# Kernel optimization log

Measured on AMD Instinct MI355X. Metric: run time of the kernel, lower is better.

The kernel has to match this reference:

```python
import jax, jax.numpy as jnp
import numpy as np

EMBED_DIM = 128
N_HEADS = 8
HEAD_DEPTH = EMBED_DIM // N_HEADS  # 16
CLIP = 10.0
B, N = 256, 1000


def setup_inputs() -> dict:
    key = jax.random.key(0)
    ks = jax.random.split(key, 10)
    D = EMBED_DIM
    return {
        "node_embeddings": jax.random.normal(ks[0], (B, N, D), jnp.float32),
        "graph_embedding": jax.random.normal(ks[1], (B, D), jnp.float32),
        "step_context": jax.random.normal(ks[2], (B, 1, D + 2), jnp.float32),
        "mask": jax.random.randint(ks[3], (B, 1, N), 0, 2).astype(bool),
        "Wk1": jax.random.normal(ks[4], (D, D), jnp.float32) / np.sqrt(D),
        "Wv": jax.random.normal(ks[5], (D, D), jnp.float32) / np.sqrt(D),
        "Wk2": jax.random.normal(ks[6], (D, D), jnp.float32) / np.sqrt(D),
        "Wq_fixed": jax.random.normal(ks[7], (D, D), jnp.float32) / np.sqrt(D),
        "Wout": jax.random.normal(ks[8], (D, D), jnp.float32) / np.sqrt(D),
        "Wq_step": jax.random.normal(ks[9], (D + 2, D), jnp.float32) / np.sqrt(D),
    }


def reference(node_embeddings, graph_embedding, step_context, mask,
              Wk1, Wv, Wk2, Wq_fixed, Wout, Wq_step):
    b, n, D = node_embeddings.shape
    H, dh = N_HEADS, HEAD_DEPTH
    neg_inf = jnp.float32(-1e9)

    # compute_static: precomputed projections of node/graph embeddings
    K1 = node_embeddings @ Wk1                      # [B,N,D]
    V = node_embeddings @ Wv                        # [B,N,D]
    K2 = node_embeddings @ Wk2                      # [B,N,D]
    Q_fixed = graph_embedding[:, None, :] @ Wq_fixed  # [B,1,D]

    # compute_dynamic: single-query masked MHA
    Q_step = step_context @ Wq_step                 # [B,1,D]
    Q1 = Q_fixed + Q_step                           # [B,1,D]
    q = Q1.reshape(b, 1, H, dh)
    k = K1.reshape(b, n, H, dh)
    v = V.reshape(b, n, H, dh)
    score = jnp.einsum('bqhd,bkhd->bhqk', q, k) / jnp.sqrt(jnp.float32(dh))
    score = jnp.where(mask[:, None, :, :], neg_inf, score)  # mask [B,1,N] -> [B,1,1,N]
    attn = jax.nn.softmax(score, axis=-1)           # [B,H,1,N]
    mha = jnp.einsum('bhqk,bkhd->bqhd', attn, v).reshape(b, 1, D)
    Q2 = mha @ Wout                                 # [B,1,D]

    # SHA: clipped single-head logits over all nodes
    logits = CLIP * jnp.tanh(
        jnp.einsum('bqd,bkd->bqk', Q2, K2) / jnp.sqrt(jnp.float32(D)))  # [B,1,N]
    logits = jnp.where(mask, neg_inf, logits)
    return logits[:, 0, :]                          # [B,N]
```

## Files before the change

### kernel.cpp

```cpp
#include <hip/hip_runtime.h>
#include <hip/hip_bf16.h>
#include <stdint.h>


#define DD 128
#define NH 8
#define DHD 16
#define NS 16
#define TILE 64
#define RP 132
#define NMAX_PAD 1024

typedef short v8s __attribute__((ext_vector_type(8)));
typedef float v4f __attribute__((ext_vector_type(4)));
typedef unsigned int v2u __attribute__((ext_vector_type(2)));

__device__ __forceinline__ unsigned short f2bf(float x) {
    unsigned u = __float_as_uint(x);
    u += 0x7fffu + ((u >> 16) & 1u);
    return (unsigned short)(u >> 16);
}
__device__ __forceinline__ float bf2f(unsigned short s) {
    return __uint_as_float((unsigned)s << 16);
}
__device__ __forceinline__ unsigned packbf2(float x, float y) {
    union { __hip_bfloat162 h; unsigned u; } cvt;
    cvt.h = __float22bfloat162_rn(make_float2(x, y));
    return cvt.u;
}

__device__ __forceinline__ v2u ds_tr16(unsigned addr) {
    v2u r;
    asm volatile("ds_read_b64_tr_b16 %0, %1" : "=v"(r) : "v"(addr));
    return r;
}
__device__ __forceinline__ v8s combine8(v2u lo, v2u hi) {
    union { struct { v2u lo, hi; } p; v8s v; } u;
    u.p.lo = lo; u.p.hi = hi;
    return u.v;
}

__device__ __forceinline__ bool detect_mask32(const void* maskp) {
    const uint32_t* mw = (const uint32_t*)maskp;
    bool m32 = true;
    #pragma unroll
    for (int i = 0; i < 16; ++i) m32 = m32 && (mw[i] <= 1u);
    return m32;
}

__global__ __launch_bounds__(128)
void k0_prep(const float* __restrict__ graph, const float* __restrict__ ctx,
             const float* __restrict__ Wk1, const float* __restrict__ Wqf,
             const float* __restrict__ Wqs, float* __restrict__ wq_ws)
{
    __shared__ float q1[DD];
    const int b = blockIdx.x, tid = threadIdx.x;
    const float* ge = graph + (size_t)b * DD;
    const float* sc = ctx + (size_t)b * (DD + 2);
    float acc = 0.f;
    #pragma unroll 4
    for (int k = 0; k < DD; ++k)     acc += ge[k] * Wqf[k * DD + tid];
    #pragma unroll 4
    for (int k = 0; k < DD + 2; ++k) acc += sc[k] * Wqs[k * DD + tid];
    q1[tid] = acc;
    __syncthreads();
    const float* wrow = Wk1 + (size_t)tid * DD;
    #pragma unroll
    for (int h = 0; h < NH; ++h) {
        float a = 0.f;
        #pragma unroll
        for (int j = 0; j < DHD; ++j) a += wrow[h * DHD + j] * q1[h * DHD + j];
        wq_ws[(size_t)b * NH * DD + h * DD + tid] = 0.25f * a;
    }
}

__global__ __launch_bounds__(256)
void kA_mfma(const float* __restrict__ node, const float* __restrict__ wq_ws,
             const void* __restrict__ maskp, unsigned short* __restrict__ spart_ws,
             float* __restrict__ mz_ws, int N)
{
    __shared__ __align__(16) unsigned short tA[8][TILE][16];
    __shared__ __align__(16) unsigned short Ph[16][72];
    __shared__ float wmax[16][5];
    __shared__ float zpart[16][5];

    const int b = blockIdx.y, j = blockIdx.x, tid = threadIdx.x;
    const int lane = tid & 63, w = tid >> 6;
    const int c = lane & 15, g = lane >> 4;
    const int rows = (N + NS - 1) / NS;
    const int n0 = j * rows;
    const int nend = min(n0 + rows, N);

    if (nend <= n0) {
        unsigned short* sp = spart_ws + ((size_t)b * NS + j) * NH * DD;
        for (int o = tid; o < NH * DD; o += 256) sp[o] = 0;
        if (tid < NH) {
            float* mzp = mz_ws + (((size_t)b * NS + j) * NH + tid) * 2;
            mzp[0] = -1e30f; mzp[1] = 0.f;
        }
        return;
    }

    const float* nodeB = node + (size_t)b * N * DD;

    const int L = tid >> 2, q = tid & 3;
    {
        const int n = n0 + L;
        const bool valid = n < nend;
        const int srcrow = valid ? n : (nend - 1);
        const float4* src = (const float4*)(nodeB + (size_t)srcrow * DD + q * 32);
        float4 f[8];
        #pragma unroll
        for (int k = 0; k < 8; ++k) f[k] = src[k];
        if (!valid) {
            #pragma unroll
            for (int k = 0; k < 8; ++k) f[k] = make_float4(0.f, 0.f, 0.f, 0.f);
        }
        union { unsigned u[16]; v8s v[4]; } pk;
        #pragma unroll
        for (int k = 0; k < 8; ++k) {
            pk.u[2 * k]     = packbf2(f[k].x, f[k].y);
            pk.u[2 * k + 1] = packbf2(f[k].z, f[k].w);
        }
        *(v8s*)&tA[2 * q][L][0]     = pk.v[0];
        *(v8s*)&tA[2 * q][L][8]     = pk.v[1];
        *(v8s*)&tA[2 * q + 1][L][0] = pk.v[2];
        *(v8s*)&tA[2 * q + 1][L][8] = pk.v[3];
    }

    v8s aw[4];
    #pragma unroll
    for (int kk = 0; kk < 4; ++kk) {
        v8s a;
        #pragma unroll
        for (int i = 0; i < 8; ++i) a[i] = 0;
        if (c < NH) {
            const float* wr = wq_ws + (size_t)b * NH * DD + (size_t)c * DD + kk * 32 + g * 8;
            #pragma unroll
            for (int i = 0; i < 8; ++i) a[i] = (short)f2bf(wr[i]);
        }
        aw[kk] = a;
    }

    const bool m32 = detect_mask32(maskp);
    const int32_t* mi = (const int32_t*)maskp + (size_t)b * N;
    const uint8_t* mb = (const uint8_t*)maskp + (size_t)b * N;

    __syncthreads();

    const int nrow = n0 + w * 16 + c;
    v4f sc = {0.f, 0.f, 0.f, 0.f};
    #pragma unroll
    for (int kk = 0; kk < 4; ++kk) {
        const v8s bfrag = *(const v8s*)&tA[2 * kk + (g >> 1)][w * 16 + c][(g & 1) * 8];
        sc = __builtin_amdgcn_mfma_f32_16x16x32_bf16(aw[kk], bfrag, sc, 0, 0, 0);
    }

    float s4[4];
    {
        const bool valid = nrow < nend;
        const bool msk = valid && (m32 ? (mi[nrow] != 0) : (mb[nrow] != 0));
        #pragma unroll
        for (int r = 0; r < 4; ++r)
            s4[r] = !valid ? -1e30f : (msk ? -1e9f : sc[r]);
    }

    {
        float mx[4];
        #pragma unroll
        for (int r = 0; r < 4; ++r) mx[r] = s4[r];
        #pragma unroll
        for (int d = 1; d < 16; d <<= 1) {
            #pragma unroll
            for (int r = 0; r < 4; ++r) mx[r] = fmaxf(mx[r], __shfl_xor(mx[r], d));
        }
        if (c == 0) {
            #pragma unroll
            for (int r = 0; r < 4; ++r) wmax[g * 4 + r][w] = mx[r];
        }
    }
    __syncthreads();

    {
        float e4[4];
        #pragma unroll
        for (int r = 0; r < 4; ++r) {
            const int h = g * 4 + r;
            const float m = fmaxf(fmaxf(wmax[h][0], wmax[h][1]),
                                  fmaxf(wmax[h][2], wmax[h][3]));
            e4[r] = __expf(s4[r] - m);
        }
        float zr[4];
        #pragma unroll
        for (int r = 0; r < 4; ++r) zr[r] = e4[r];
        #pragma unroll
        for (int d = 1; d < 16; d <<= 1) {
            #pragma unroll
            for (int r = 0; r < 4; ++r) zr[r] += __shfl_xor(zr[r], d);
        }
        if (c == 0) {
            #pragma unroll
            for (int r = 0; r < 4; ++r) zpart[g * 4 + r][w] = zr[r];
        }
        #pragma unroll
        for (int r = 0; r < 4; ++r)
            Ph[g * 4 + r][w * 16 + c] = f2bf(e4[r]);
    }
    __syncthreads();

    const unsigned tAbase  = (unsigned)(size_t)&tA[0][0][0];
    const unsigned laneoff = (unsigned)(g * 256 + c * 2);
    v2u tr[8];
    #pragma unroll
    for (int sl = 0; sl < 2; ++sl) {
        #pragma unroll
        for (int chk = 0; chk < 2; ++chk) {
            #pragma unroll
            for (int hf = 0; hf < 2; ++hf) {
                const unsigned a = tAbase + (unsigned)((2 * w + chk) * 2048 + sl * 1024 + hf * 128) + laneoff;
                tr[sl * 4 + chk * 2 + hf] = ds_tr16(a);
            }
        }
    }
    asm volatile("s_waitcnt lgkmcnt(0)" ::: "memory");
    __builtin_amdgcn_sched_barrier(0);

    v4f c0 = {0.f, 0.f, 0.f, 0.f}, c1 = {0.f, 0.f, 0.f, 0.f};
    #pragma unroll
    for (int sl = 0; sl < 2; ++sl) {
        const v8s pa  = *(const v8s*)&Ph[c][sl * 32 + g * 8];
        const v8s bb0 = combine8(tr[sl * 4 + 0], tr[sl * 4 + 1]);
        const v8s bb1 = combine8(tr[sl * 4 + 2], tr[sl * 4 + 3]);
        c0 = __builtin_amdgcn_mfma_f32_16x16x32_bf16(pa, bb0, c0, 0, 0, 0);
        c1 = __builtin_amdgcn_mfma_f32_16x16x32_bf16(pa, bb1, c1, 0, 0, 0);
    }

    if (g < 2) {
        unsigned short* sp = spart_ws + ((size_t)b * NS + j) * NH * DD;
        #pragma unroll
        for (int r = 0; r < 4; ++r) {
            sp[(g * 4 + r) * DD + (2 * w)     * 16 + c] = f2bf(c0[r]);
            sp[(g * 4 + r) * DD + (2 * w + 1) * 16 + c] = f2bf(c1[r]);
        }
    }
    if (tid < NH) {
        const float z = zpart[tid][0] + zpart[tid][1] + zpart[tid][2] + zpart[tid][3];
        const float m = fmaxf(fmaxf(wmax[tid][0], wmax[tid][1]),
                              fmaxf(wmax[tid][2], wmax[tid][3]));
        float* mzp = mz_ws + (((size_t)b * NS + j) * NH + tid) * 2;
        mzp[0] = m;
        mzp[1] = z;
    }
}

__global__ __launch_bounds__(128)
void kB_combine(const unsigned short* __restrict__ spart_ws, const float* __restrict__ mz_ws,
                const float* __restrict__ Wv, const float* __restrict__ Wout,
                const float* __restrict__ Wk2, float* __restrict__ w2_ws)
{
    __shared__ float m_l[NH * NS], z_l[NH * NS], wt[NH * NS];
    __shared__ float s_l[NH * DD];
    __shared__ float mha_l[DD];
    __shared__ float q2_l[DD];
    const int b = blockIdx.x, tid = threadIdx.x;

    {
        const int h = tid >> 4, j = tid & 15;
        const float* mzp = mz_ws + (((size_t)b * NS + j) * NH + h) * 2;
        m_l[h * NS + j] = mzp[0];
        z_l[h * NS + j] = mzp[1];
    }
    __syncthreads();
    if (tid < NH) {
        const int h = tid;
        float M = -1e30f;
        #pragma unroll
        for (int j = 0; j < NS; ++j) M = fmaxf(M, m_l[h * NS + j]);
        float Z = 0.f;
        float wv[NS];
        #pragma unroll
        for (int j = 0; j < NS; ++j) {
            wv[j] = __expf(m_l[h * NS + j] - M);
            Z += z_l[h * NS + j] * wv[j];
        }
        const float rz = 1.f / Z;
        #pragma unroll
        for (int j = 0; j < NS; ++j) wt[h * NS + j] = wv[j] * rz;
    }
    __syncthreads();
    const unsigned short* sp = spart_ws + (size_t)b * NS * NH * DD;
    for (int o = tid; o < NH * DD; o += 128) {
        const int h = o >> 7;
        float s = 0.f;
        #pragma unroll
        for (int j = 0; j < NS; ++j)
            s += bf2f(sp[(size_t)j * NH * DD + o]) * wt[h * NS + j];
        s_l[o] = s;
    }
    __syncthreads();
    {
        const int h = tid >> 4;
        float a = 0.f;
        for (int dp = 0; dp < DD; ++dp) a += s_l[h * DD + dp] * Wv[dp * DD + tid];
        mha_l[tid] = a;
    }
    __syncthreads();
    {
        float a = 0.f;
        for (int e = 0; e < DD; ++e) a += mha_l[e] * Wout[e * DD + tid];
        q2_l[tid] = a;
    }
    __syncthreads();
    {
        const float4* row = (const float4*)(Wk2 + (size_t)tid * DD);
        float a = 0.f;
        #pragma unroll
        for (int k = 0; k < 32; ++k) {
            const float4 w = row[k];
            a += w.x * q2_l[4*k] + w.y * q2_l[4*k+1] + w.z * q2_l[4*k+2] + w.w * q2_l[4*k+3];
        }
        w2_ws[(size_t)b * DD + tid] = a * 0.08838834764831845f;
    }
}

__global__ __launch_bounds__(256)
void k5_logits(const float* __restrict__ node, const float* __restrict__ w2_ws,
               const void* __restrict__ maskp, float* __restrict__ out, int N)
{
    const int b = blockIdx.y, j = blockIdx.x, tid = threadIdx.x;
    const int rows = (N + NS - 1) / NS;
    const int n0 = j * rows;
    const int nend = min(n0 + rows, N);
    const bool m32 = detect_mask32(maskp);
    const int32_t* mi = (const int32_t*)maskp + (size_t)b * N;
    const uint8_t* mb = (const uint8_t*)maskp + (size_t)b * N;
    const int sub = tid & 7, rr = tid >> 3;

    const float4* wv = (const float4*)(w2_ws + (size_t)b * DD + sub * 16);
    const float4 w0 = wv[0], w1 = wv[1], w2v = wv[2], w3 = wv[3];
    const float* nodeB = node + (size_t)b * N * DD;
    float* outB = out + (size_t)b * N;

    for (int n = n0 + rr; n < nend; n += 32) {
        const float4* nr = (const float4*)(nodeB + (size_t)n * DD + sub * 16);
        const float4 a0 = nr[0], a1 = nr[1], a2 = nr[2], a3 = nr[3];
        float p = a0.x*w0.x + a0.y*w0.y + a0.z*w0.z + a0.w*w0.w
                + a1.x*w1.x + a1.y*w1.y + a1.z*w1.z + a1.w*w1.w
                + a2.x*w2v.x + a2.y*w2v.y + a2.z*w2v.z + a2.w*w2v.w
                + a3.x*w3.x + a3.y*w3.y + a3.z*w3.z + a3.w*w3.w;
        p += __shfl_xor(p, 1);
        p += __shfl_xor(p, 2);
        p += __shfl_xor(p, 4);
        if (sub == 0) {
            const bool m = m32 ? (mi[n] != 0) : (mb[n] != 0);
            const float t = 1.f - 2.f / (__expf(2.f * p) + 1.f);
            outB[n] = m ? -1e9f : 10.f * t;
        }
    }
}

#define TPB 512
#define NMAX 1000
#define SPAD 9

__global__ __launch_bounds__(TPB)
void decoder_fallback(const float* __restrict__ node, const float* __restrict__ graph,
                      const float* __restrict__ ctx, const void* __restrict__ maskp,
                      const float* __restrict__ Wk1, const float* __restrict__ Wv,
                      const float* __restrict__ Wk2, const float* __restrict__ Wqf,
                      const float* __restrict__ Wout, const float* __restrict__ Wqs,
                      float* __restrict__ out, int N)
{
    __shared__ float node_tile[TILE * RP];
    __shared__ float scores[NMAX * SPAD];
    __shared__ float wq[NH * RP];
    __shared__ float s_lds[NH * RP];
    __shared__ float q1[DD];
    __shared__ float mha[DD];
    __shared__ float q2[DD];
    __shared__ float w2[DD];

    const int b = blockIdx.x, tid = threadIdx.x, lane = tid & 63, wave = tid >> 6;
    const bool mask32 = detect_mask32(maskp);
    const int32_t* mi = (const int32_t*)maskp + (size_t)b * N;
    const uint8_t* mb = (const uint8_t*)maskp + (size_t)b * N;
    const float* nodeB = node + (size_t)b * N * DD;

    if (tid < DD) {
        const float* ge = graph + (size_t)b * DD;
        const float* sc = ctx + (size_t)b * (DD + 2);
        float acc = 0.f;
        for (int k = 0; k < DD; ++k)     acc += ge[k] * Wqf[k * DD + tid];
        for (int k = 0; k < DD + 2; ++k) acc += sc[k] * Wqs[k * DD + tid];
        q1[tid] = acc;
    }
    __syncthreads();
    for (int idx = tid; idx < NH * DD; idx += TPB) {
        const int h = idx >> 7, dp = idx & (DD - 1);
        const float* wrow = Wk1 + dp * DD + h * DHD;
        float acc = 0.f;
        #pragma unroll
        for (int j = 0; j < DHD; ++j) acc += wrow[j] * q1[h * DHD + j];
        wq[h * RP + dp] = 0.25f * acc;
    }
    __syncthreads();
    const int ntiles = (N + TILE - 1) / TILE;
    const int n_local = tid >> 3, hA = tid & 7;
    for (int t = 0; t < ntiles; ++t) {
        const int n0 = t * TILE;
        #pragma unroll
        for (int cc = 0; cc < 4; ++cc) {
            const int idx = cc * (TPB * 4) + tid * 4;
            const int row = idx >> 7, col = idx & (DD - 1);
            if (n0 + row < N)
                *(float4*)&node_tile[row * RP + col] =
                    *(const float4*)(nodeB + (size_t)(n0 + row) * DD + col);
        }
        __syncthreads();
        if (n0 + n_local < N) {
            const float4* nr = (const float4*)&node_tile[n_local * RP];
            const float4* wr = (const float4*)&wq[hA * RP];
            float acc = 0.f;
            #pragma unroll
            for (int k = 0; k < DD / 4; ++k) {
                const float4 a = nr[k], wv = wr[k];
                acc += a.x * wv.x + a.y * wv.y + a.z * wv.z + a.w * wv.w;
            }
            scores[(n0 + n_local) * SPAD + hA] = acc;
        }
        __syncthreads();
    }
    {
        const int h = wave;
        float sm[16];
        #pragma unroll
        for (int k = 0; k < 16; ++k) {
            const int n = lane + 64 * k;
            float v = -1e9f;
            if (n < N) {
                const bool m = mask32 ? (mi[n] != 0) : (mb[n] != 0);
                v = m ? -1e9f : scores[n * SPAD + h];
            }
            sm[k] = v;
        }
        float mx = sm[0];
        #pragma unroll
        for (int k = 1; k < 16; ++k) mx = fmaxf(mx, sm[k]);
        #pragma unroll
        for (int d = 1; d < 64; d <<= 1) mx = fmaxf(mx, __shfl_xor(mx, d));
        float e[16];
        float sum = 0.f;
        #pragma unroll
        for (int k = 0; k < 16; ++k) {
            const int n = lane + 64 * k;
            e[k] = (n < N) ? __expf(sm[k] - mx) : 0.f;
            sum += e[k];
        }
        #pragma unroll
        for (int d = 1; d < 64; d <<= 1) sum += __shfl_xor(sum, d);
        const float rinv = 1.f / sum;
        #pragma unroll
        for (int k = 0; k < 16; ++k) {
            const int n = lane + 64 * k;
            if (n < N) scores[n * SPAD + h] = e[k] * rinv;
        }
    }
    __syncthreads();
    {
        const int h = wave;
        const float2* n2 = (const float2*)nodeB;
        float a0 = 0.f, a1 = 0.f;
        #pragma unroll 4
        for (int n = 0; n < N; ++n) {
            const float at = scores[n * SPAD + h];
            const float2 v = n2[(size_t)n * 64 + lane];
            a0 += at * v.x;
            a1 += at * v.y;
        }
        s_lds[h * RP + 2 * lane] = a0;
        s_lds[h * RP + 2 * lane + 1] = a1;
    }
    __syncthreads();
    if (tid < DD) {
        const int h = tid >> 4;
        float acc = 0.f;
        for (int dp = 0; dp < DD; ++dp) acc += s_lds[h * RP + dp] * Wv[dp * DD + tid];
        mha[tid] = acc;
    }
    __syncthreads();
    if (tid < DD) {
        float acc = 0.f;
        for (int e = 0; e < DD; ++e) acc += mha[e] * Wout[e * DD + tid];
        q2[tid] = acc;
    }
    __syncthreads();
    if (tid < DD) {
        const float4* row = (const float4*)(Wk2 + tid * DD);
        float acc = 0.f;
        #pragma unroll
        for (int k = 0; k < DD / 4; ++k) {
            const float4 wv = row[k];
            acc += wv.x * q2[4*k] + wv.y * q2[4*k+1] + wv.z * q2[4*k+2] + wv.w * q2[4*k+3];
        }
        w2[tid] = acc * 0.08838834764831845f;
    }
    __syncthreads();
    {
        const float wa = w2[2 * lane], wb = w2[2 * lane + 1];
        const float2* n2 = (const float2*)nodeB;
        float* outB = out + (size_t)b * N;
        for (int n = wave; n < N; n += NH) {
            const float2 v = n2[(size_t)n * 64 + lane];
            float p = v.x * wa + v.y * wb;
            #pragma unroll
            for (int d = 1; d < 64; d <<= 1) p += __shfl_xor(p, d);
            if (lane == 0) {
                const bool m = mask32 ? (mi[n] != 0) : (mb[n] != 0);
                const float t = 1.f - 2.f / (__expf(2.f * p) + 1.f);
                outB[n] = m ? -1e9f : 10.f * t;
            }
        }
    }
}

extern "C" void kernel_launch(void* const* d_in, const int* in_sizes, int n_in,
                              void* d_out, int out_size, void* d_ws, size_t ws_size,
                              hipStream_t stream) {
    (void)n_in; (void)out_size;
    const float* node  = (const float*)d_in[0];
    const float* graph = (const float*)d_in[1];
    const float* ctx   = (const float*)d_in[2];
    const void*  mask  = d_in[3];
    const float* Wk1   = (const float*)d_in[4];
    const float* Wv    = (const float*)d_in[5];
    const float* Wk2   = (const float*)d_in[6];
    const float* Wqf   = (const float*)d_in[7];
    const float* Wout  = (const float*)d_in[8];
    const float* Wqs   = (const float*)d_in[9];

    const int B = in_sizes[1] / DD;
    const int N = in_sizes[0] / (B * DD);

    const size_t wq_bytes    = (size_t)B * NH * DD * 4;
    const size_t spart_bytes = (size_t)B * NS * NH * DD * 2;
    const size_t mz_bytes    = (size_t)B * NS * NH * 2 * 4;
    const size_t w2_bytes    = (size_t)B * DD * 4;
    const size_t need_bytes  = wq_bytes + spart_bytes + mz_bytes + w2_bytes;

    if (N <= NMAX_PAD && ws_size >= need_bytes) {
        char* ws = (char*)d_ws;
        float*          wq_ws    = (float*)ws;
        unsigned short* spart_ws = (unsigned short*)(ws + wq_bytes);
        float*          mz_ws    = (float*)(ws + wq_bytes + spart_bytes);
        float*          w2_ws    = (float*)(ws + wq_bytes + spart_bytes + mz_bytes);

        k0_prep<<<B, 128, 0, stream>>>(graph, ctx, Wk1, Wqf, Wqs, wq_ws);
        kA_mfma<<<dim3(NS, B), 256, 0, stream>>>(node, wq_ws, mask, spart_ws, mz_ws, N);
        kB_combine<<<B, 128, 0, stream>>>(spart_ws, mz_ws, Wv, Wout, Wk2, w2_ws);
        k5_logits<<<dim3(NS, B), 256, 0, stream>>>(node, w2_ws, mask, (float*)d_out, N);
    } else {
        decoder_fallback<<<B, TPB, 0, stream>>>(node, graph, ctx, mask,
                                                Wk1, Wv, Wk2, Wqf, Wout, Wqs,
                                                (float*)d_out, N);
    }
}
```

Baseline: 98.41 us.

## Fuse four kernels into two, recomputing per-batch prep in every block

Folds the query-projection prep kernel into the attention MFMA kernel and the combine kernel into the logits kernel, so each of the 16 blocks per batch recomputes the small per-batch projections redundantly instead of passing them through workspace. This removes two launches and their global round-trips, at the cost of duplicated matrix-vector work per block. It also replaces the ds_read_b64_tr_b16 transpose reads with scalar LDS gathers for the B fragment.

```diff
diff --git a/kernel.cpp b/kernel.cpp
--- a/kernel.cpp
+++ b/kernel.cpp
@@ -13,7 +13,6 @@
 
 typedef short v8s __attribute__((ext_vector_type(8)));
 typedef float v4f __attribute__((ext_vector_type(4)));
-typedef unsigned int v2u __attribute__((ext_vector_type(2)));
 
 __device__ __forceinline__ unsigned short f2bf(float x) {
     unsigned u = __float_as_uint(x);
@@ -27,17 +26,6 @@
     union { __hip_bfloat162 h; unsigned u; } cvt;
     cvt.h = __float22bfloat162_rn(make_float2(x, y));
     return cvt.u;
-}
-
-__device__ __forceinline__ v2u ds_tr16(unsigned addr) {
-    v2u r;
-    asm volatile("ds_read_b64_tr_b16 %0, %1" : "=v"(r) : "v"(addr));
-    return r;
-}
-__device__ __forceinline__ v8s combine8(v2u lo, v2u hi) {
-    union { struct { v2u lo, hi; } p; v8s v; } u;
-    u.p.lo = lo; u.p.hi = hi;
-    return u.v;
 }
 
 __device__ __forceinline__ bool detect_mask32(const void* maskp) {
@@ -48,39 +36,17 @@
     return m32;
 }
 
-__global__ __launch_bounds__(128)
-void k0_prep(const float* __restrict__ graph, const float* __restrict__ ctx,
-             const float* __restrict__ Wk1, const float* __restrict__ Wqf,
-             const float* __restrict__ Wqs, float* __restrict__ wq_ws)
-{
-    __shared__ float q1[DD];
-    const int b = blockIdx.x, tid = threadIdx.x;
-    const float* ge = graph + (size_t)b * DD;
-    const float* sc = ctx + (size_t)b * (DD + 2);
-    float acc = 0.f;
-    #pragma unroll 4
-    for (int k = 0; k < DD; ++k)     acc += ge[k] * Wqf[k * DD + tid];
-    #pragma unroll 4
-    for (int k = 0; k < DD + 2; ++k) acc += sc[k] * Wqs[k * DD + tid];
-    q1[tid] = acc;
-    __syncthreads();
-    const float* wrow = Wk1 + (size_t)tid * DD;
-    #pragma unroll
-    for (int h = 0; h < NH; ++h) {
-        float a = 0.f;
-        #pragma unroll
-        for (int j = 0; j < DHD; ++j) a += wrow[h * DHD + j] * q1[h * DHD + j];
-        wq_ws[(size_t)b * NH * DD + h * DD + tid] = 0.25f * a;
-    }
-}
-
 __global__ __launch_bounds__(256)
-void kA_mfma(const float* __restrict__ node, const float* __restrict__ wq_ws,
-             const void* __restrict__ maskp, unsigned short* __restrict__ spart_ws,
-             float* __restrict__ mz_ws, int N)
+void kA_fused(const float* __restrict__ node, const float* __restrict__ graph,
+              const float* __restrict__ ctx, const float* __restrict__ Wk1,
+              const float* __restrict__ Wqf, const float* __restrict__ Wqs,
+              const void* __restrict__ maskp, unsigned short* __restrict__ spart_ws,
+              float* __restrict__ mz_ws, int N)
 {
     __shared__ __align__(16) unsigned short tA[8][TILE][16];
+    __shared__ __align__(16) unsigned short wqb[16][DD];
     __shared__ __align__(16) unsigned short Ph[16][72];
+    __shared__ float q1[DD];
     __shared__ float wmax[16][5];
     __shared__ float zpart[16][5];
 
@@ -128,18 +94,29 @@
         *(v8s*)&tA[2 * q + 1][L][8] = pk.v[3];
     }
 
-    v8s aw[4];
-    #pragma unroll
-    for (int kk = 0; kk < 4; ++kk) {
-        v8s a;
-        #pragma unroll
-        for (int i = 0; i < 8; ++i) a[i] = 0;
-        if (c < NH) {
-            const float* wr = wq_ws + (size_t)b * NH * DD + (size_t)c * DD + kk * 32 + g * 8;
-            #pragma unroll
-            for (int i = 0; i < 8; ++i) a[i] = (short)f2bf(wr[i]);
-        }
-        aw[kk] = a;
+    if (tid < DD) {
+        const float* ge = graph + (size_t)b * DD;
+        const float* sc = ctx + (size_t)b * (DD + 2);
+        float acc = 0.f;
+        #pragma unroll 4
+        for (int k = 0; k < DD; ++k)     acc += ge[k] * Wqf[k * DD + tid];
+        #pragma unroll 4
+        for (int k = 0; k < DD + 2; ++k) acc += sc[k] * Wqs[k * DD + tid];
+        q1[tid] = acc;
+    }
+    __syncthreads();
+
+    for (int idx = tid; idx < 16 * DD; idx += 256) {
+        const int h = idx >> 7, dp = idx & 127;
+        unsigned short v = 0;
+        if (h < NH) {
+            const float* wrow = Wk1 + (size_t)dp * DD + h * DHD;
+            float a = 0.f;
+            #pragma unroll
+            for (int j2 = 0; j2 < DHD; ++j2) a += wrow[j2] * q1[h * DHD + j2];
+            v = f2bf(0.25f * a);
+        }
+        wqb[h][dp] = v;
     }
 
     const bool m32 = detect_mask32(maskp);
@@ -147,6 +124,11 @@
     const uint8_t* mb = (const uint8_t*)maskp + (size_t)b * N;
 
     __syncthreads();
+
+    v8s aw[4];
+    #pragma unroll
+    for (int kk = 0; kk < 4; ++kk)
+        aw[kk] = *(const v8s*)&wqb[c][kk * 32 + g * 8];
 
     const int nrow = n0 + w * 16 + c;
     v4f sc = {0.f, 0.f, 0.f, 0.f};
@@ -208,29 +190,17 @@
     }
     __syncthreads();
 
-    const unsigned tAbase  = (unsigned)(size_t)&tA[0][0][0];
-    const unsigned laneoff = (unsigned)(g * 256 + c * 2);
-    v2u tr[8];
-    #pragma unroll
-    for (int sl = 0; sl < 2; ++sl) {
-        #pragma unroll
-        for (int chk = 0; chk < 2; ++chk) {
-            #pragma unroll
-            for (int hf = 0; hf < 2; ++hf) {
-                const unsigned a = tAbase + (unsigned)((2 * w + chk) * 2048 + sl * 1024 + hf * 128) + laneoff;
-                tr[sl * 4 + chk * 2 + hf] = ds_tr16(a);
-            }
-        }
-    }
-    asm volatile("s_waitcnt lgkmcnt(0)" ::: "memory");
-    __builtin_amdgcn_sched_barrier(0);
-
     v4f c0 = {0.f, 0.f, 0.f, 0.f}, c1 = {0.f, 0.f, 0.f, 0.f};
     #pragma unroll
     for (int sl = 0; sl < 2; ++sl) {
-        const v8s pa  = *(const v8s*)&Ph[c][sl * 32 + g * 8];
-        const v8s bb0 = combine8(tr[sl * 4 + 0], tr[sl * 4 + 1]);
-        const v8s bb1 = combine8(tr[sl * 4 + 2], tr[sl * 4 + 3]);
+        const v8s pa = *(const v8s*)&Ph[c][sl * 32 + g * 8];
+        v8s bb0, bb1;
+        #pragma unroll
+        for (int i = 0; i < 8; ++i) {
+            const int kr = sl * 32 + g * 8 + i;
+            bb0[i] = (short)tA[2 * w][kr][c];
+            bb1[i] = (short)tA[2 * w + 1][kr][c];
+        }
         c0 = __builtin_amdgcn_mfma_f32_16x16x32_bf16(pa, bb0, c0, 0, 0, 0);
         c1 = __builtin_amdgcn_mfma_f32_16x16x32_bf16(pa, bb1, c1, 0, 0, 0);
     }
@@ -253,81 +223,78 @@
     }
 }
 
-__global__ __launch_bounds__(128)
-void kB_combine(const unsigned short* __restrict__ spart_ws, const float* __restrict__ mz_ws,
-                const float* __restrict__ Wv, const float* __restrict__ Wout,
-                const float* __restrict__ Wk2, float* __restrict__ w2_ws)
+__global__ __launch_bounds__(256)
+void kBC_fused(const float* __restrict__ node, const unsigned short* __restrict__ spart_ws,
+               const float* __restrict__ mz_ws, const float* __restrict__ Wv,
+               const float* __restrict__ Wout, const float* __restrict__ Wk2,
+               const void* __restrict__ maskp, float* __restrict__ out, int N)
 {
     __shared__ float m_l[NH * NS], z_l[NH * NS], wt[NH * NS];
     __shared__ float s_l[NH * DD];
     __shared__ float mha_l[DD];
     __shared__ float q2_l[DD];
-    const int b = blockIdx.x, tid = threadIdx.x;
-
-    {
-        const int h = tid >> 4, j = tid & 15;
-        const float* mzp = mz_ws + (((size_t)b * NS + j) * NH + h) * 2;
-        m_l[h * NS + j] = mzp[0];
-        z_l[h * NS + j] = mzp[1];
+    __shared__ __align__(16) float w2_l[DD];
+    const int b = blockIdx.y, j = blockIdx.x, tid = threadIdx.x;
+
+    if (tid < NH * NS) {
+        const int h = tid >> 4, jj = tid & 15;
+        const float* mzp = mz_ws + (((size_t)b * NS + jj) * NH + h) * 2;
+        m_l[h * NS + jj] = mzp[0];
+        z_l[h * NS + jj] = mzp[1];
     }
     __syncthreads();
     if (tid < NH) {
         const int h = tid;
         float M = -1e30f;
         #pragma unroll
-        for (int j = 0; j < NS; ++j) M = fmaxf(M, m_l[h * NS + j]);
+        for (int jj = 0; jj < NS; ++jj) M = fmaxf(M, m_l[h * NS + jj]);
         float Z = 0.f;
         float wv[NS];
         #pragma unroll
-        for (int j = 0; j < NS; ++j) {
-            wv[j] = __expf(m_l[h * NS + j] - M);
-            Z += z_l[h * NS + j] * wv[j];
+        for (int jj = 0; jj < NS; ++jj) {
+            wv[jj] = __expf(m_l[h * NS + jj] - M);
+            Z += z_l[h * NS + jj] * wv[jj];
         }
         const float rz = 1.f / Z;
         #pragma unroll
-        for (int j = 0; j < NS; ++j) wt[h * NS + j] = wv[j] * rz;
+        for (int jj = 0; jj < NS; ++jj) wt[h * NS + jj] = wv[jj] * rz;
     }
     __syncthreads();
     const unsigned short* sp = spart_ws + (size_t)b * NS * NH * DD;
-    for (int o = tid; o < NH * DD; o += 128) {
+    for (int o = tid; o < NH * DD; o += 256) {
         const int h = o >> 7;
         float s = 0.f;
         #pragma unroll
-        for (int j = 0; j < NS; ++j)
-            s += bf2f(sp[(size_t)j * NH * DD + o]) * wt[h * NS + j];
+        for (int jj = 0; jj < NS; ++jj)
+            s += bf2f(sp[(size_t)jj * NH * DD + o]) * wt[h * NS + jj];
         s_l[o] = s;
     }
     __syncthreads();
-    {
+    if (tid < DD) {
         const int h = tid >> 4;
         float a = 0.f;
         for (int dp = 0; dp < DD; ++dp) a += s_l[h * DD + dp] * Wv[dp * DD + tid];
         mha_l[tid] = a;
     }
     __syncthreads();
-    {
+    if (tid < DD) {
         float a = 0.f;
         for (int e = 0; e < DD; ++e) a += mha_l[e] * Wout[e * DD + tid];
         q2_l[tid] = a;
     }
     __syncthreads();
-    {
+    if (tid < DD) {
         const float4* row = (const float4*)(Wk2 + (size_t)tid * DD);
         float a = 0.f;
         #pragma unroll
         for (int k = 0; k < 32; ++k) {
-            const float4 w = row[k];
-            a += w.x * q2_l[4*k] + w.y * q2_l[4*k+1] + w.z * q2_l[4*k+2] + w.w * q2_l[4*k+3];
-        }
-        w2_ws[(size_t)b * DD + tid] = a * 0.08838834764831845f;
-    }
-}
-
-__global__ __launch_bounds__(256)
-void k5_logits(const float* __restrict__ node, const float* __restrict__ w2_ws,
-               const void* __restrict__ maskp, float* __restrict__ out, int N)
-{
-    const int b = blockIdx.y, j = blockIdx.x, tid = threadIdx.x;
+            const float4 wv = row[k];
+            a += wv.x * q2_l[4*k] + wv.y * q2_l[4*k+1] + wv.z * q2_l[4*k+2] + wv.w * q2_l[4*k+3];
+        }
+        w2_l[tid] = a * 0.08838834764831845f;
+    }
+    __syncthreads();
+
     const int rows = (N + NS - 1) / NS;
     const int n0 = j * rows;
     const int nend = min(n0 + rows, N);
@@ -336,8 +303,8 @@
     const uint8_t* mb = (const uint8_t*)maskp + (size_t)b * N;
     const int sub = tid & 7, rr = tid >> 3;
 
-    const float4* wv = (const float4*)(w2_ws + (size_t)b * DD + sub * 16);
-    const float4 w0 = wv[0], w1 = wv[1], w2v = wv[2], w3 = wv[3];
+    const float4* wv4 = (const float4*)&w2_l[sub * 16];
+    const float4 w0 = wv4[0], w1 = wv4[1], w2v = wv4[2], w3 = wv4[3];
     const float* nodeB = node + (size_t)b * N * DD;
     float* outB = out + (size_t)b * N;
 
@@ -541,23 +508,19 @@
     const int B = in_sizes[1] / DD;
     const int N = in_sizes[0] / (B * DD);
 
-    const size_t wq_bytes    = (size_t)B * NH * DD * 4;
     const size_t spart_bytes = (size_t)B * NS * NH * DD * 2;
     const size_t mz_bytes    = (size_t)B * NS * NH * 2 * 4;
-    const size_t w2_bytes    = (size_t)B * DD * 4;
-    const size_t need_bytes  = wq_bytes + spart_bytes + mz_bytes + w2_bytes;
+    const size_t need_bytes  = spart_bytes + mz_bytes;
 
     if (N <= NMAX_PAD && ws_size >= need_bytes) {
         char* ws = (char*)d_ws;
-        float*          wq_ws    = (float*)ws;
-        unsigned short* spart_ws = (unsigned short*)(ws + wq_bytes);
-        float*          mz_ws    = (float*)(ws + wq_bytes + spart_bytes);
-        float*          w2_ws    = (float*)(ws + wq_bytes + spart_bytes + mz_bytes);
-
-        k0_prep<<<B, 128, 0, stream>>>(graph, ctx, Wk1, Wqf, Wqs, wq_ws);
-        kA_mfma<<<dim3(NS, B), 256, 0, stream>>>(node, wq_ws, mask, spart_ws, mz_ws, N);
-        kB_combine<<<B, 128, 0, stream>>>(spart_ws, mz_ws, Wv, Wout, Wk2, w2_ws);
-        k5_logits<<<dim3(NS, B), 256, 0, stream>>>(node, w2_ws, mask, (float*)d_out, N);
+        unsigned short* spart_ws = (unsigned short*)ws;
+        float*          mz_ws    = (float*)(ws + spart_bytes);
+
+        kA_fused<<<dim3(NS, B), 256, 0, stream>>>(node, graph, ctx, Wk1, Wqf, Wqs,
+                                                  mask, spart_ws, mz_ws, N);
+        kBC_fused<<<dim3(NS, B), 256, 0, stream>>>(node, spart_ws, mz_ws, Wv, Wout, Wk2,
+                                                   mask, (float*)d_out, N);
     } else {
         decoder_fallback<<<B, TPB, 0, stream>>>(node, graph, ctx, mask,
                                                 Wk1, Wv, Wk2, Wqf, Wout, Wqs,
```

Measured after the change: 191.5 us. +94.6%, slower.
